# Kernel tuning notes

Hardware: AMD Instinct MI355X
Metric: run time of the kernel (lower is better)

Reference implementation:

```python
import jax, jax.numpy as jnp
import numpy as np

N_SITES = 64   # number of sampled indices (n = 2**6 in source)
CHI = 64       # virtual bond dimension of the isometric TN
BATCH = 32768  # number of independent perfect samples


def _isometrize(W):
    """Right-canonical isometrization (analog of mera.isometrize(method='cayley')).

    W: [n, chi, 2, chi] raw params -> A with sum_{s,r} A[l,s,r] A[l',s,r] = delta_{ll'}.
    """
    n, chi = W.shape[0], W.shape[1]
    M = W.reshape(n, chi, 2 * chi)               # [n, chi, 2*chi]
    Q, _ = jnp.linalg.qr(jnp.swapaxes(M, 1, 2))  # [n, 2*chi, chi], orthonormal columns
    return jnp.swapaxes(Q, 1, 2).reshape(n, chi, 2, chi)


def setup_inputs() -> dict:
    key = jax.random.key(0)
    k1, k2 = jax.random.split(key)
    W = jax.random.normal(k1, (N_SITES, CHI, 2, CHI), dtype=jnp.float32)
    u = jax.random.uniform(k2, (BATCH, N_SITES), dtype=jnp.float32)
    return {"W": W, "u": u}


def reference(W, u):
    """Perfect (autoregressive exact-conditional) sampling from an isometric TN.

    Returns:
      s_hat: [B, n, 2] one-hot samples, outcome 0 -> [0,1], outcome 1 -> [1,0]
             (matching v0=[0,1], v1=[1,0] in the source)
      prob:  [B, n] conditional probability of the drawn outcome at each step
             (the `probability` array the source maintains).
    """
    A = _isometrize(W)                 # [n, chi, 2, chi]
    B, n = u.shape
    chi = W.shape[1]
    # left boundary environment (unit norm) -> total norm is exactly 1
    L0 = jnp.zeros((B, chi), dtype=W.dtype).at[:, 0].set(1.0)

    def step(L, inp):
        A_i, u_i = inp                              # [chi,2,chi], [B]
        T = jnp.einsum('bl,lsr->bsr', L, A_i)       # [B, 2, chi]
        p = jnp.sum(T * T, axis=-1)                 # [B, 2]; p0 + p1 == 1 by isometry
        take1 = u_i >= p[:, 0]                      # r < ps0 -> outcome 0
        s = take1.astype(jnp.int32)
        p_s = jnp.where(take1, p[:, 1], p[:, 0])    # probability of chosen branch
        T_s = jnp.where(take1[:, None], T[:, 1, :], T[:, 0, :])
        L_new = T_s / jnp.sqrt(p_s)[:, None]        # renormalize by sqrt(prob)
        return L_new, (s, p_s)

    _, (s, p) = jax.lax.scan(step, L0, (A, u.T))    # s,p: [n, B]
    s = s.T                                         # [B, n]
    prob = p.T                                      # [B, n]
    s_hat = jax.nn.one_hot(1 - s, 2, dtype=W.dtype)  # 0 -> [0,1], 1 -> [1,0]
    return s_hat, prob
```

## Files before the change

kernel.cpp:

```cpp
#include <hip/hip_runtime.h>

#define NSITES 64
#define CHI 64
#define BATCH 32768
#define LPAD 66

typedef double d4 __attribute__((ext_vector_type(4)));

#define MFMA_HAZARD_FENCE() do {                                    \
    __builtin_amdgcn_sched_barrier(0);                              \
    asm volatile("s_nop 7\n\ts_nop 7\n\ts_nop 7\n\ts_nop 7" :::);   \
    __builtin_amdgcn_sched_barrier(0);                              \
} while (0)

__global__ __launch_bounds__(512) void qr_site_kernel(
    const float* __restrict__ W, double* __restrict__ A8)
{
    __shared__ double M[128][65];
    __shared__ double wpart[8][64];
    __shared__ double tauS[64];
    __shared__ double scS[64];
    __shared__ double redS2[8];
    __shared__ double Vt[64][136];

    const int i   = blockIdx.x;
    const int tid = threadIdx.x;

    for (int idx = tid; idx < 8192; idx += 512) {
        int l = idx >> 7, sr = idx & 127;
        M[sr][l] = (double)W[i * 8192 + idx];
    }

    const int jf = tid & 63;
    const int gf = tid >> 6;
    const int r0 = gf * 16;
    __syncthreads();

    for (int k = 0; k < 64; ++k) {
        double ureg[16];
        #pragma unroll
        for (int m = 0; m < 16; ++m) {
            int rr = r0 + m;
            ureg[m] = (rr > k) ? M[rr][k] : 0.0;
        }
        double np = 0.0;
        #pragma unroll
        for (int m = 0; m < 16; ++m) np = fma(ureg[m], ureg[m], np);
        if (jf == 0) redS2[gf] = np;
        if (jf > k) {
            double part = 0.0;
            #pragma unroll 4
            for (int m = 0; m < 16; ++m)
                part = fma(ureg[m], M[r0 + m][jf], part);
            wpart[gf][jf] = part;
        }
        __syncthreads();

        const double v2 = ((redS2[0] + redS2[1]) + (redS2[2] + redS2[3]))
                        + ((redS2[4] + redS2[5]) + (redS2[6] + redS2[7]));
        const double alpha = M[k][k];
        double beta, tk;
        if (v2 == 0.0) { beta = alpha; tk = 0.0; }
        else {
            double nrm = sqrt(alpha * alpha + v2);
            beta = (alpha >= 0.0) ? -nrm : nrm;
            tk   = (beta - alpha) / beta;
        }
        const double uk   = alpha - beta;
        const double sc   = (tk != 0.0) ? (1.0 / uk) : 0.0;
        const double tau2 = (tk != 0.0) ? (tk / (uk * uk)) : 0.0;
        if (tid == 0) { tauS[k] = tk; scS[k] = sc; }
        if (jf > k) {
            const double xk = M[k][jf];
            double wsum = ((wpart[0][jf] + wpart[1][jf]) + (wpart[2][jf] + wpart[3][jf]))
                        + ((wpart[4][jf] + wpart[5][jf]) + (wpart[6][jf] + wpart[7][jf]));
            const double wj = tau2 * fma(uk, xk, wsum);
            #pragma unroll 4
            for (int m = 0; m < 16; ++m) {
                int rr = r0 + m;
                M[rr][jf] = fma(-ureg[m], wj, M[rr][jf]);
            }
        }
        __syncthreads();
    }

    for (int idx = tid; idx < 8192; idx += 512) {
        int rr = idx & 127, k = idx >> 7;
        double val = (rr > k) ? M[rr][k] * scS[k] : ((rr == k) ? 1.0 : 0.0);
        Vt[k][rr + (rr >> 4)] = val;
    }
    __syncthreads();

    const int jq = tid >> 3;
    const int qq = tid & 7;
    double E[16];
    #pragma unroll
    for (int m = 0; m < 16; ++m) E[m] = ((qq * 16 + m) == jq) ? 1.0 : 0.0;

    for (int k = 63; k >= 0; --k) {
        const double tkk = tauS[k];
        double part = 0.0;
        #pragma unroll
        for (int m = 0; m < 16; ++m) {
            int rr = qq * 16 + m;
            part = fma(Vt[k][rr + qq], E[m], part);
        }
        part += __shfl_xor(part, 1, 64);
        part += __shfl_xor(part, 2, 64);
        part += __shfl_xor(part, 4, 64);
        const double wj = tkk * part;
        #pragma unroll
        for (int m = 0; m < 16; ++m) {
            int rr = qq * 16 + m;
            E[m] = fma(-Vt[k][rr + qq], wj, E[m]);
        }
    }

    double* dst = A8 + (size_t)i * 8192 + jq * 128 + qq * 16;
    #pragma unroll
    for (int m = 0; m < 16; ++m) dst[m] = E[m];
}

#define MFMA_ROW(bp, a)                                                   \
    c0 = __builtin_amdgcn_mfma_f64_16x16x4f64((a), (bp)[  0], c0, 0,0,0); \
    c1 = __builtin_amdgcn_mfma_f64_16x16x4f64((a), (bp)[ 16], c1, 0,0,0); \
    c2 = __builtin_amdgcn_mfma_f64_16x16x4f64((a), (bp)[ 32], c2, 0,0,0); \
    c3 = __builtin_amdgcn_mfma_f64_16x16x4f64((a), (bp)[ 48], c3, 0,0,0); \
    c4 = __builtin_amdgcn_mfma_f64_16x16x4f64((a), (bp)[ 64], c4, 0,0,0); \
    c5 = __builtin_amdgcn_mfma_f64_16x16x4f64((a), (bp)[ 80], c5, 0,0,0); \
    c6 = __builtin_amdgcn_mfma_f64_16x16x4f64((a), (bp)[ 96], c6, 0,0,0); \
    c7 = __builtin_amdgcn_mfma_f64_16x16x4f64((a), (bp)[112], c7, 0,0,0);

__global__ __launch_bounds__(512, 2) void sample_kernel(
    const double* __restrict__ A8, const float* __restrict__ u,
    float* __restrict__ out)
{
    __shared__ __align__(16) double As[8192];
    __shared__ double Lsm[128 * LPAD];

    const int tid  = threadIdx.x;
    const int w    = tid >> 6;
    const int lane = tid & 63;
    const int g    = lane >> 4;
    const int r    = lane & 15;
    const int ubase = blockIdx.x * 128 + 16 * w;

    d4 zp = {0.0, 0.0, 0.0, 0.0};
    const d4 rowP = __builtin_amdgcn_mfma_f64_16x16x4f64((g == 0) ? (double)r : 0.0, 1.0, zp, 0, 0, 0);
    const d4 colP = __builtin_amdgcn_mfma_f64_16x16x4f64((g == 0) ? 1.0 : 0.0, (double)r, zp, 0, 0, 0);
    MFMA_HAZARD_FENCE();
    const int row0 = (int)(rowP.x + 0.5), row1 = (int)(rowP.y + 0.5);
    const int row2 = (int)(rowP.z + 0.5), row3 = (int)(rowP.w + 0.5);
    const int col0 = (int)(colP.x + 0.5), col1 = (int)(colP.y + 0.5);
    const int col2 = (int)(colP.z + 0.5), col3 = (int)(colP.w + 0.5);

    for (int j = g; j < 64; j += 4)
        Lsm[(16 * w + r) * LPAD + j] = (j == 0) ? 1.0 : 0.0;

    {
        const double2* s2 = (const double2*)A8;
        double2* a2 = (double2*)As;
        #pragma unroll
        for (int q = 0; q < 8; ++q) a2[q * 512 + tid] = s2[q * 512 + tid];
    }
    __syncthreads();

    float* probOut = out + (size_t)BATCH * (NSITES * 2);

    for (int site = 0; site < NSITES; ++site) {
        const float u0 = u[(size_t)(ubase + row0) * NSITES + site];
        const float u1 = u[(size_t)(ubase + row1) * NSITES + site];
        const float u2 = u[(size_t)(ubase + row2) * NSITES + site];
        const float u3 = u[(size_t)(ubase + row3) * NSITES + site];

        double2 st0, st1, st2, st3;
        if (site < NSITES - 1) {
            const double2* nx = (const double2*)(A8 + (size_t)(site + 1) * 8192);
            st0 = nx[0 * 512 + tid]; st1 = nx[1 * 512 + tid];
            st2 = nx[2 * 512 + tid]; st3 = nx[3 * 512 + tid];
        }

        d4 c0 = {0.0, 0.0, 0.0, 0.0}, c1 = c0, c2 = c0, c3 = c0;
        d4 c4 = c0, c5 = c0, c6 = c0, c7 = c0;

        const double* Lp = Lsm + (16 * w + r) * LPAD + g;
        const double* Ap = As + g * 128 + r;

        #pragma unroll
        for (int kk = 0; kk < 8; ++kk) {
            const double a = Lp[4 * kk];
            const double* bp = Ap + kk * 512;
            MFMA_ROW(bp, a)
        }

        __syncthreads();

        double2 st4, st5, st6, st7;
        if (site < NSITES - 1) {
            double2* a2 = (double2*)As;
            a2[0 * 512 + tid] = st0; a2[1 * 512 + tid] = st1;
            a2[2 * 512 + tid] = st2; a2[3 * 512 + tid] = st3;
            const double2* nx = (const double2*)(A8 + (size_t)(site + 1) * 8192);
            st4 = nx[4 * 512 + tid]; st5 = nx[5 * 512 + tid];
            st6 = nx[6 * 512 + tid]; st7 = nx[7 * 512 + tid];
        }

        #pragma unroll
        for (int kk = 8; kk < 16; ++kk) {
            const double a = Lp[4 * kk];
            const double* bp = Ap + kk * 512;
            MFMA_ROW(bp, a)
        }

        __syncthreads();

        MFMA_HAZARD_FENCE();

        double P0 = fma(c3.x, c3.x, fma(c2.x, c2.x, fma(c1.x, c1.x, c0.x * c0.x)));
        double P1 = fma(c3.y, c3.y, fma(c2.y, c2.y, fma(c1.y, c1.y, c0.y * c0.y)));
        double P2 = fma(c3.z, c3.z, fma(c2.z, c2.z, fma(c1.z, c1.z, c0.z * c0.z)));
        double P3 = fma(c3.w, c3.w, fma(c2.w, c2.w, fma(c1.w, c1.w, c0.w * c0.w)));
        #pragma unroll
        for (int m = 1; m <= 8; m <<= 1) {
            P0 += __shfl_xor(P0, m, 64);
            P1 += __shfl_xor(P1, m, 64);
            P2 += __shfl_xor(P2, m, 64);
            P3 += __shfl_xor(P3, m, 64);
        }

        const bool t0 = ((double)u0 >= P0);
        const bool t1 = ((double)u1 >= P1);
        const bool t2 = ((double)u2 >= P2);
        const bool t3 = ((double)u3 >= P3);
        const double s0 = t0 ? (1.0 - P0) : P0;
        const double s1 = t1 ? (1.0 - P1) : P1;
        const double s2 = t2 ? (1.0 - P2) : P2;
        const double s3 = t3 ? (1.0 - P3) : P3;
        const double i0 = rsqrt(s0);
        const double i1 = rsqrt(s1);
        const double i2 = rsqrt(s2);
        const double i3 = rsqrt(s3);

        double* LwB = Lsm + (16 * w) * LPAD;
        LwB[row0 * LPAD +  0 + col0] = (t0 ? c4.x : c0.x) * i0;
        LwB[row0 * LPAD + 16 + col0] = (t0 ? c5.x : c1.x) * i0;
        LwB[row0 * LPAD + 32 + col0] = (t0 ? c6.x : c2.x) * i0;
        LwB[row0 * LPAD + 48 + col0] = (t0 ? c7.x : c3.x) * i0;
        LwB[row1 * LPAD +  0 + col1] = (t1 ? c4.y : c0.y) * i1;
        LwB[row1 * LPAD + 16 + col1] = (t1 ? c5.y : c1.y) * i1;
        LwB[row1 * LPAD + 32 + col1] = (t1 ? c6.y : c2.y) * i1;
        LwB[row1 * LPAD + 48 + col1] = (t1 ? c7.y : c3.y) * i1;
        LwB[row2 * LPAD +  0 + col2] = (t2 ? c4.z : c0.z) * i2;
        LwB[row2 * LPAD + 16 + col2] = (t2 ? c5.z : c1.z) * i2;
        LwB[row2 * LPAD + 32 + col2] = (t2 ? c6.z : c2.z) * i2;
        LwB[row2 * LPAD + 48 + col2] = (t2 ? c7.z : c3.z) * i2;
        LwB[row3 * LPAD +  0 + col3] = (t3 ? c4.w : c0.w) * i3;
        LwB[row3 * LPAD + 16 + col3] = (t3 ? c5.w : c1.w) * i3;
        LwB[row3 * LPAD + 32 + col3] = (t3 ? c6.w : c2.w) * i3;
        LwB[row3 * LPAD + 48 + col3] = (t3 ? c7.w : c3.w) * i3;

        if (r == 0) {
            probOut[(size_t)(ubase + row0) * NSITES + site] = (float)s0;
            probOut[(size_t)(ubase + row1) * NSITES + site] = (float)s1;
            probOut[(size_t)(ubase + row2) * NSITES + site] = (float)s2;
            probOut[(size_t)(ubase + row3) * NSITES + site] = (float)s3;
            *(float2*)(out + (size_t)(ubase + row0) * 128 + site * 2) = make_float2(t0 ? 1.f : 0.f, t0 ? 0.f : 1.f);
            *(float2*)(out + (size_t)(ubase + row1) * 128 + site * 2) = make_float2(t1 ? 1.f : 0.f, t1 ? 0.f : 1.f);
            *(float2*)(out + (size_t)(ubase + row2) * 128 + site * 2) = make_float2(t2 ? 1.f : 0.f, t2 ? 0.f : 1.f);
            *(float2*)(out + (size_t)(ubase + row3) * 128 + site * 2) = make_float2(t3 ? 1.f : 0.f, t3 ? 0.f : 1.f);
        }

        if (site < NSITES - 1) {
            double2* a2 = (double2*)As;
            a2[4 * 512 + tid] = st4; a2[5 * 512 + tid] = st5;
            a2[6 * 512 + tid] = st6; a2[7 * 512 + tid] = st7;
        }
    }
}

extern "C" void kernel_launch(void* const* d_in, const int* in_sizes, int n_in,
                              void* d_out, int out_size, void* d_ws, size_t ws_size,
                              hipStream_t stream)
{
    const float* W = (const float*)d_in[0];
    const float* u = (const float*)d_in[1];
    float* out = (float*)d_out;
    double* A8 = (double*)d_ws;

    hipLaunchKernelGGL(qr_site_kernel, dim3(NSITES), dim3(512), 0, stream, W, A8);
    hipLaunchKernelGGL(sample_kernel, dim3(256), dim3(512), 0, stream, A8, u, out);
}
```

Measured before the change: 764.6 us.

## Read site tensors directly from global memory instead of staging through LDS

Removes the LDS staging and double-buffered prefetch of each site's A tensor. MFMA B operands are now loaded straight from global memory, which should hit L2 since every block reads the same data. This drops the two block barriers per site and the 64KB LDS buffer. Blocks shrink to 256 threads and the grid doubles to 512, raising occupancy and removing cross-wave synchronisation, at the cost of more global/L2 load traffic and exposed load latency per MFMA.

```diff
diff --git a/kernel.cpp b/kernel.cpp
--- a/kernel.cpp
+++ b/kernel.cpp
@@ -131,19 +131,18 @@
     c6 = __builtin_amdgcn_mfma_f64_16x16x4f64((a), (bp)[ 96], c6, 0,0,0); \
     c7 = __builtin_amdgcn_mfma_f64_16x16x4f64((a), (bp)[112], c7, 0,0,0);
 
-__global__ __launch_bounds__(512, 2) void sample_kernel(
+__global__ __launch_bounds__(256, 2) void sample_kernel(
     const double* __restrict__ A8, const float* __restrict__ u,
     float* __restrict__ out)
 {
-    __shared__ __align__(16) double As[8192];
-    __shared__ double Lsm[128 * LPAD];
+    __shared__ double Lsm[64 * LPAD];
 
     const int tid  = threadIdx.x;
     const int w    = tid >> 6;
     const int lane = tid & 63;
     const int g    = lane >> 4;
     const int r    = lane & 15;
-    const int ubase = blockIdx.x * 128 + 16 * w;
+    const int ubase = blockIdx.x * 64 + 16 * w;
 
     d4 zp = {0.0, 0.0, 0.0, 0.0};
     const d4 rowP = __builtin_amdgcn_mfma_f64_16x16x4f64((g == 0) ? (double)r : 0.0, 1.0, zp, 0, 0, 0);
@@ -157,14 +156,6 @@
     for (int j = g; j < 64; j += 4)
         Lsm[(16 * w + r) * LPAD + j] = (j == 0) ? 1.0 : 0.0;
 
-    {
-        const double2* s2 = (const double2*)A8;
-        double2* a2 = (double2*)As;
-        #pragma unroll
-        for (int q = 0; q < 8; ++q) a2[q * 512 + tid] = s2[q * 512 + tid];
-    }
-    __syncthreads();
-
     float* probOut = out + (size_t)BATCH * (NSITES * 2);
 
     for (int site = 0; site < NSITES; ++site) {
@@ -173,47 +164,18 @@
         const float u2 = u[(size_t)(ubase + row2) * NSITES + site];
         const float u3 = u[(size_t)(ubase + row3) * NSITES + site];
 
-        double2 st0, st1, st2, st3;
-        if (site < NSITES - 1) {
-            const double2* nx = (const double2*)(A8 + (size_t)(site + 1) * 8192);
-            st0 = nx[0 * 512 + tid]; st1 = nx[1 * 512 + tid];
-            st2 = nx[2 * 512 + tid]; st3 = nx[3 * 512 + tid];
-        }
-
         d4 c0 = {0.0, 0.0, 0.0, 0.0}, c1 = c0, c2 = c0, c3 = c0;
         d4 c4 = c0, c5 = c0, c6 = c0, c7 = c0;
 
         const double* Lp = Lsm + (16 * w + r) * LPAD + g;
-        const double* Ap = As + g * 128 + r;
-
-        #pragma unroll
-        for (int kk = 0; kk < 8; ++kk) {
+        const double* Ab = A8 + (size_t)site * 8192 + g * 128 + r;
+
+        #pragma unroll
+        for (int kk = 0; kk < 16; ++kk) {
             const double a = Lp[4 * kk];
-            const double* bp = Ap + kk * 512;
+            const double* bp = Ab + kk * 512;
             MFMA_ROW(bp, a)
         }
-
-        __syncthreads();
-
-        double2 st4, st5, st6, st7;
-        if (site < NSITES - 1) {
-            double2* a2 = (double2*)As;
-            a2[0 * 512 + tid] = st0; a2[1 * 512 + tid] = st1;
-            a2[2 * 512 + tid] = st2; a2[3 * 512 + tid] = st3;
-            const double2* nx = (const double2*)(A8 + (size_t)(site + 1) * 8192);
-            st4 = nx[4 * 512 + tid]; st5 = nx[5 * 512 + tid];
-            st6 = nx[6 * 512 + tid]; st7 = nx[7 * 512 + tid];
-        }
-
-        #pragma unroll
-        for (int kk = 8; kk < 16; ++kk) {
-            const double a = Lp[4 * kk];
-            const double* bp = Ap + kk * 512;
-            MFMA_ROW(bp, a)
-        }
-
-        __syncthreads();
-
         MFMA_HAZARD_FENCE();
 
         double P0 = fma(c3.x, c3.x, fma(c2.x, c2.x, fma(c1.x, c1.x, c0.x * c0.x)));
@@ -269,12 +231,6 @@
             *(float2*)(out + (size_t)(ubase + row2) * 128 + site * 2) = make_float2(t2 ? 1.f : 0.f, t2 ? 0.f : 1.f);
             *(float2*)(out + (size_t)(ubase + row3) * 128 + site * 2) = make_float2(t3 ? 1.f : 0.f, t3 ? 0.f : 1.f);
         }
-
-        if (site < NSITES - 1) {
-            double2* a2 = (double2*)As;
-            a2[4 * 512 + tid] = st4; a2[5 * 512 + tid] = st5;
-            a2[6 * 512 + tid] = st6; a2[7 * 512 + tid] = st7;
-        }
     }
 }
 
@@ -288,5 +244,5 @@
     double* A8 = (double*)d_ws;
 
     hipLaunchKernelGGL(qr_site_kernel, dim3(NSITES), dim3(512), 0, stream, W, A8);
-    hipLaunchKernelGGL(sample_kernel, dim3(256), dim3(512), 0, stream, A8, u, out);
+    hipLaunchKernelGGL(sample_kernel, dim3(512), dim3(256), 0, stream, A8, u, out);
 }
```

Measured after the change: 1.357 ms. 77.5% more time.
